# Kernel tuning notes

Measured on AMD Instinct MI355X. Metric: run time of the kernel, lower is better.

The kernel has to match this reference:

```python
import math
import jax, jax.numpy as jnp
import numpy as np

HEADS = 8
D_MODEL = 256


def positional_encoding_2d(c, h, w):
    # faithful port of wzlxjtu/PositionalEncoding2D
    d = c // 2
    div_term = jnp.exp(jnp.arange(0.0, d, 2, dtype=jnp.float32) * (-(math.log(10000.0) / d)))  # [d//2? no: d/2 entries -> d//2]
    pos_w = jnp.arange(0.0, w, dtype=jnp.float32)[:, None] * div_term  # [w, d//2]
    pos_h = jnp.arange(0.0, h, dtype=jnp.float32)[:, None] * div_term  # [h, d//2]
    pe = jnp.zeros((c, h, w), dtype=jnp.float32)
    sw = jnp.broadcast_to(jnp.sin(pos_w).T[:, None, :], (div_term.shape[0], h, w))
    cw = jnp.broadcast_to(jnp.cos(pos_w).T[:, None, :], (div_term.shape[0], h, w))
    sh = jnp.broadcast_to(jnp.sin(pos_h).T[:, :, None], (div_term.shape[0], h, w))
    ch = jnp.broadcast_to(jnp.cos(pos_h).T[:, :, None], (div_term.shape[0], h, w))
    pe = pe.at[0:d:2].set(sw)
    pe = pe.at[1:d:2].set(cw)
    pe = pe.at[d::2].set(sh)
    pe = pe.at[d + 1::2].set(ch)
    return pe


def setup_inputs() -> dict:
    key = jax.random.key(0)
    ks = jax.random.split(key, 9)
    b, c, h, w = 2, D_MODEL, 64, 64
    x = jax.random.normal(ks[0], (b, c, h, w), dtype=jnp.float32)
    s = 0.02
    Wq = jax.random.normal(ks[1], (c, c), dtype=jnp.float32) * s
    Wk = jax.random.normal(ks[2], (c, c), dtype=jnp.float32) * s
    Wv = jax.random.normal(ks[3], (c, c), dtype=jnp.float32) * s
    Wo = jax.random.normal(ks[4], (c, c), dtype=jnp.float32) * s
    bq = jax.random.normal(ks[5], (c,), dtype=jnp.float32) * s
    bk = jax.random.normal(ks[6], (c,), dtype=jnp.float32) * s
    bv = jax.random.normal(ks[7], (c,), dtype=jnp.float32) * s
    bo = jax.random.normal(ks[8], (c,), dtype=jnp.float32) * s
    return {"x": x, "Wq": Wq, "bq": bq, "Wk": Wk, "bk": bk,
            "Wv": Wv, "bv": bv, "Wo": Wo, "bo": bo}


def reference(x, Wq, bq, Wk, bk, Wv, bv, Wo, bo):
    b, c, h, w = x.shape
    dk = c // HEADS
    pe = positional_encoding_2d(c, h, w)
    x2 = x + pe[None]                                   # [b,c,h,w]
    tok = x2.reshape(b, c, h * w).transpose(0, 2, 1)    # [b,N,c]
    q = (tok @ Wq.T + bq).reshape(b, -1, HEADS, dk).transpose(0, 2, 1, 3)  # [b,H,N,dk]
    k = (tok @ Wk.T + bk).reshape(b, -1, HEADS, dk).transpose(0, 2, 1, 3)
    v = (tok @ Wv.T + bv).reshape(b, -1, HEADS, dk).transpose(0, 2, 1, 3)
    scores = jnp.einsum('bhnd,bhmd->bhnm', q, k) / math.sqrt(dk)  # [b,H,N,N]
    attn = jax.nn.softmax(scores, axis=-1)
    out = jnp.einsum('bhnm,bhmd->bhnd', attn, v)        # [b,H,N,dk]
    concat = out.transpose(0, 2, 1, 3).reshape(b, -1, c)  # [b,N,c]
    proj = concat @ Wo.T + bo                           # [b,N,c]
    return proj.transpose(0, 2, 1).reshape(b, c, h, w)
```

## Files before the change

### kernel.cpp

```cpp
#include <hip/hip_runtime.h>
#include <hip/hip_bf16.h>
#include <cstdint>

typedef float f32x4 __attribute__((ext_vector_type(4)));
typedef __bf16 bf16x8 __attribute__((ext_vector_type(8)));
typedef uint32_t uint2v __attribute__((ext_vector_type(2)));

#define MFMA_K32(A, B, C) __builtin_amdgcn_mfma_f32_16x16x32_bf16((A), (B), (C), 0, 0, 0)

#if __has_builtin(__builtin_amdgcn_exp2f)
#define EXP2(x) __builtin_amdgcn_exp2f(x)
#else
#define EXP2(x) exp2f(x)
#endif

static __device__ __forceinline__ uint16_t f2b(float f) {
    uint32_t u = __float_as_uint(f);
    uint32_t r = (u + 0x7fffu + ((u >> 16) & 1u)) >> 16;
    return (uint16_t)r;
}

static __device__ __forceinline__ uint32_t packbf(float a, float b) {
    uint32_t r;
    asm("v_cvt_pk_bf16_f32 %0, %1, %2" : "=v"(r) : "v"(a), "v"(b));
    return r;
}

__global__ __launch_bounds__(512) void prep(const float* __restrict__ x,
                                            const float* __restrict__ wq,
                                            const float* __restrict__ wk,
                                            const float* __restrict__ wv,
                                            const float* __restrict__ wo,
                                            uint16_t* __restrict__ dst,
                                            uint16_t* __restrict__ tok) {
    __shared__ uint16_t T[64][65];
    int tid = threadIdx.x, bid = blockIdx.x;
    if (bid < 512) {
        int nt = bid & 63, ct = (bid >> 6) & 3, bb = bid >> 8;
        int n0 = nt << 6, c0 = ct << 6;
        int nl = tid & 63, cq = tid >> 6;
        int n = n0 + nl;
        float pf = (float)((c0 & 128) ? nt : nl);
        int cbase = c0 + cq * 8;
        int ibase = (cbase & 127) >> 1;
        float dt = __expf((float)(2 * ibase) * -0.07195578415606394f);
#pragma unroll
        for (int j = 0; j < 4; ++j) {
            float sv, cv;
            __sincosf(pf * dt, &sv, &cv);
            int cl = cq * 8 + 2 * j;
            int cc = cbase + 2 * j;
            T[cl][nl]     = f2b(x[((size_t)(bb * 256 + cc) << 12) + n] + sv);
            T[cl + 1][nl] = f2b(x[((size_t)(bb * 256 + cc + 1) << 12) + n] + cv);
            dt *= 0.8659643233600653f;
        }
        __syncthreads();
#pragma unroll
        for (int p = 0; p < 8; ++p) {
            int tl = cq * 8 + p;
            tok[(((size_t)(bb << 12) | (n0 + tl)) << 8) + c0 + nl] = T[nl][tl];
        }
    } else {
        int idx = (bid - 512) * 512 + tid;
        int which = idx >> 16, off = idx & 65535;
        const float* s = (which == 0) ? wq : (which == 1) ? wk : (which == 2) ? wv : wo;
        dst[idx] = f2b(s[off]);
    }
}

__global__ __launch_bounds__(256) void qkv_gemm(const uint16_t* __restrict__ tok,
                                                const uint16_t* __restrict__ Wall,
                                                const float* __restrict__ bq,
                                                const float* __restrict__ bk,
                                                const float* __restrict__ bv,
                                                uint16_t* __restrict__ qo,
                                                uint16_t* __restrict__ ko,
                                                uint16_t* __restrict__ vo) {
    __shared__ __align__(16) uint16_t WS[64][264];
    int tid = threadIdx.x, wv = tid >> 6, lane = tid & 63;
    int c16 = lane & 15, quad = lane >> 4;
    int M0 = blockIdx.x * 64 + wv * 16;
    int O0 = blockIdx.y * 64;
    const uint16_t* arow = tok + (size_t)(M0 + c16) * 256;
    bf16x8 af[8];
#pragma unroll
    for (int kk = 0; kk < 8; ++kk) af[kk] = *(const bf16x8*)(arow + kk * 32 + quad * 8);
    f32x4 zero = {0.f, 0.f, 0.f, 0.f};
    int bb = M0 >> 12, n = (M0 + c16) & 4095;
    int srow = tid >> 5, sch = (tid & 31) << 3;
    for (int mat = 0; mat < 3; ++mat) {
        const uint16_t* Wg = Wall + (size_t)mat * 65536 + (size_t)O0 * 256;
        __syncthreads();
#pragma unroll
        for (int p = 0; p < 8; ++p)
            *(bf16x8*)(&WS[p * 8 + srow][sch]) = *(const bf16x8*)(Wg + (p * 8 + srow) * 256 + sch);
        __syncthreads();
        f32x4 acc[4] = {zero, zero, zero, zero};
#pragma unroll
        for (int kk = 0; kk < 8; ++kk) {
            int k0 = kk * 32 + quad * 8;
#pragma unroll
            for (int nb = 0; nb < 4; ++nb)
                acc[nb] = MFMA_K32(*(const bf16x8*)(&WS[nb * 16 + c16][k0]),
                                   af[kk], acc[nb]);
        }
        const float* bias = (mat == 0) ? bq : (mat == 1) ? bk : bv;
        if (mat < 2) {
            float scale = (mat == 0) ? 0.25505654134660127f : 1.0f;
            uint16_t* dst = (mat == 0) ? qo : ko;
#pragma unroll
            for (int nb = 0; nb < 4; ++nb) {
                int o = O0 + nb * 16 + quad * 4;
                f32x4 bi = *(const f32x4*)(bias + o);
                int h = o >> 5, dd = o & 31;
                uint2v pk;
                pk[0] = packbf((acc[nb][0] + bi[0]) * scale, (acc[nb][1] + bi[1]) * scale);
                pk[1] = packbf((acc[nb][2] + bi[2]) * scale, (acc[nb][3] + bi[3]) * scale);
                *(uint2v*)(dst + ((size_t)(bb * 8 + h) * 4096 + n) * 32 + dd) = pk;
            }
        } else {
#pragma unroll
            for (int nb = 0; nb < 4; ++nb)
#pragma unroll
                for (int r = 0; r < 4; ++r) {
                    int o = O0 + nb * 16 + quad * 4 + r;
                    vo[((size_t)(bb * 8 + (o >> 5)) * 32 + (o & 31)) * 4096 + n] =
                        f2b(acc[nb][r] + bias[o]);
                }
        }
    }
}

__global__ __launch_bounds__(512, 2) void flash(const uint16_t* __restrict__ qb,
                                                const uint16_t* __restrict__ kb,
                                                const uint16_t* __restrict__ vtb,
                                                uint16_t* __restrict__ concat) {
    __shared__ __align__(16) char smem[38912];
    int tid = threadIdx.x, wv = tid >> 6, lane = tid & 63;
    int c16 = lane & 15, quad = lane >> 4;
    int half = tid >> 8, t2 = tid & 255;
    int bh = blockIdx.y;
    int q0 = (blockIdx.x << 8) + (wv & 3) * 64;
    size_t base = (size_t)bh << 12;

    uint16_t* KT = (uint16_t*)(smem + half * 19456);
    uint16_t* VT = (uint16_t*)(smem + half * 19456 + 10240);

    const uint16_t* kgp = kb + (base + (size_t)half * 2048 + (t2 >> 2)) * 32 + (t2 & 3) * 8;
    const uint16_t* vgp = vtb + ((size_t)bh * 32 + (t2 >> 3)) * 4096 + half * 2048 + (t2 & 7) * 8;
    uint16_t* kls = KT + (t2 >> 2) * 40 + (t2 & 3) * 8;
    uint16_t* vls = VT + (t2 >> 3) * 72 + (t2 & 7) * 8;

    bf16x8 qf[4];
#pragma unroll
    for (int qbk = 0; qbk < 4; ++qbk)
        qf[qbk] = *(const bf16x8*)(qb + (base + q0 + qbk * 16 + c16) * 32 + quad * 8);

    int rbase = ((c16 >> 2) << 3) + (c16 & 3);

    union { uint32_t u[4]; bf16x8 v; } onesu;
    onesu.u[0] = 0x3F803F80u; onesu.u[1] = 0x3F803F80u;
    onesu.u[2] = 0x3F803F80u; onesu.u[3] = 0x3F803F80u;
    bf16x8 ones = onesu.v;

    f32x4 zero = {0.f, 0.f, 0.f, 0.f};
    f32x4 oA[4], oB[4], oS[4];
#pragma unroll
    for (int qbk = 0; qbk < 4; ++qbk) { oA[qbk] = zero; oB[qbk] = zero; oS[qbk] = zero; }

    {
        bf16x8 kr = *(const bf16x8*)kgp;
        bf16x8 vr = *(const bf16x8*)vgp;
        *(bf16x8*)kls = kr;
        *(bf16x8*)vls = vr;
    }
    __syncthreads();

    for (int kt = 0; kt < 32; ++kt) {
        int cur = kt & 1;
        int kn = (kt + 1) & 31;
        bf16x8 kr = *(const bf16x8*)(kgp + (size_t)kn * 2048);
        bf16x8 vr = *(const bf16x8*)(vgp + kn * 64);
        const uint16_t* kfp = KT + cur * 2560 + rbase * 40 + quad * 8;
        const uint16_t* vfp = VT + cur * 2304 + c16 * 72 + quad * 8;
        bf16x8 kf[4], vA[2], vB[2];
        kf[0] = *(const bf16x8*)(kfp);
        kf[1] = *(const bf16x8*)(kfp + 160);
        kf[2] = *(const bf16x8*)(kfp + 1280);
        kf[3] = *(const bf16x8*)(kfp + 1440);
        vA[0] = *(const bf16x8*)(vfp);
        vA[1] = *(const bf16x8*)(vfp + 32);
        vB[0] = *(const bf16x8*)(vfp + 1152);
        vB[1] = *(const bf16x8*)(vfp + 1152 + 32);

#pragma unroll
        for (int qbk = 0; qbk < 4; ++qbk) {
            f32x4 s[4];
#pragma unroll
            for (int c = 0; c < 4; ++c) s[c] = MFMA_K32(kf[c], qf[qbk], zero);
#pragma unroll
            for (int p = 0; p < 2; ++p) {
#pragma unroll
                for (int r = 0; r < 4; ++r) {
                    s[2 * p][r] = EXP2(s[2 * p][r]);
                    s[2 * p + 1][r] = EXP2(s[2 * p + 1][r]);
                }
                union { bf16x8 v; uint32_t u[4]; } pa;
                pa.u[0] = packbf(s[2 * p][0], s[2 * p][1]);
                pa.u[1] = packbf(s[2 * p][2], s[2 * p][3]);
                pa.u[2] = packbf(s[2 * p + 1][0], s[2 * p + 1][1]);
                pa.u[3] = packbf(s[2 * p + 1][2], s[2 * p + 1][3]);
                oA[qbk] = MFMA_K32(pa.v, vA[p], oA[qbk]);
                oB[qbk] = MFMA_K32(pa.v, vB[p], oB[qbk]);
                oS[qbk] = MFMA_K32(pa.v, ones, oS[qbk]);
            }
        }

        *(bf16x8*)(kls + (cur ^ 1) * 2560) = kr;
        *(bf16x8*)(vls + (cur ^ 1) * 2304) = vr;
        __syncthreads();
    }

    float* ov = (float*)smem;
    if (wv >= 4) {
        float* d = ov + ((wv - 4) * 64 + lane) * 33;
#pragma unroll
        for (int qbk = 0; qbk < 4; ++qbk)
#pragma unroll
            for (int r = 0; r < 4; ++r) {
                d[qbk * 8 + r] = oA[qbk][r];
                d[qbk * 8 + 4 + r] = oB[qbk][r];
            }
    }
    __syncthreads();
    if (wv < 4) {
        const float* s = ov + (wv * 64 + lane) * 33;
#pragma unroll
        for (int qbk = 0; qbk < 4; ++qbk)
#pragma unroll
            for (int r = 0; r < 4; ++r) {
                oA[qbk][r] += s[qbk * 8 + r];
                oB[qbk][r] += s[qbk * 8 + 4 + r];
            }
    }
    __syncthreads();
    if (wv >= 4) {
        float* d = ov + ((wv - 4) * 64 + lane) * 17;
#pragma unroll
        for (int qbk = 0; qbk < 4; ++qbk)
#pragma unroll
            for (int r = 0; r < 4; ++r) d[qbk * 4 + r] = oS[qbk][r];
    }
    __syncthreads();
    if (wv < 4) {
        const float* s = ov + (wv * 64 + lane) * 17;
        int h = bh & 7, bb = bh >> 3;
#pragma unroll
        for (int qbk = 0; qbk < 4; ++qbk)
#pragma unroll
            for (int r = 0; r < 4; ++r) {
                float l = oS[qbk][r] + s[qbk * 4 + r];
                float inv = 1.f / l;
                int n = q0 + qbk * 16 + quad * 4 + r;
                size_t row = ((size_t)bb * 4096 + n) * 256 + h * 32;
                concat[row + c16]      = f2b(oA[qbk][r] * inv);
                concat[row + 16 + c16] = f2b(oB[qbk][r] * inv);
            }
    }
}

__global__ __launch_bounds__(256) void proj_gemm(const uint16_t* __restrict__ concat,
                                                 const uint16_t* __restrict__ Wo,
                                                 const float* __restrict__ bo,
                                                 float* __restrict__ out) {
    __shared__ __align__(16) uint16_t WS[64][264];
    int tid = threadIdx.x, wv = tid >> 6, lane = tid & 63;
    int c16 = lane & 15, quad = lane >> 4;
    int M0 = blockIdx.x * 64 + wv * 16;
    int O0 = blockIdx.y * 64;
    int srow = tid >> 5, sch = (tid & 31) << 3;
    const uint16_t* Wg = Wo + (size_t)O0 * 256;
#pragma unroll
    for (int p = 0; p < 8; ++p)
        *(bf16x8*)(&WS[p * 8 + srow][sch]) = *(const bf16x8*)(Wg + (p * 8 + srow) * 256 + sch);
    const uint16_t* crow = concat + (size_t)(M0 + c16) * 256;
    bf16x8 af[8];
#pragma unroll
    for (int kk = 0; kk < 8; ++kk) af[kk] = *(const bf16x8*)(crow + kk * 32 + quad * 8);
    __syncthreads();
    f32x4 zero = {0.f, 0.f, 0.f, 0.f};
    f32x4 acc[4] = {zero, zero, zero, zero};
#pragma unroll
    for (int kk = 0; kk < 8; ++kk) {
        int k0 = kk * 32 + quad * 8;
#pragma unroll
        for (int nb = 0; nb < 4; ++nb)
            acc[nb] = MFMA_K32(*(const bf16x8*)(&WS[nb * 16 + c16][k0]),
                               af[kk], acc[nb]);
    }
    int bb = M0 >> 12, n = (M0 + c16) & 4095;
#pragma unroll
    for (int nb = 0; nb < 4; ++nb)
#pragma unroll
        for (int r = 0; r < 4; ++r) {
            int o = O0 + nb * 16 + quad * 4 + r;
            out[((size_t)(bb * 256 + o) << 12) + n] = acc[nb][r] + bo[o];
        }
}

extern "C" void kernel_launch(void* const* d_in, const int* in_sizes, int n_in,
                              void* d_out, int out_size, void* d_ws, size_t ws_size,
                              hipStream_t stream) {
    const float* x  = (const float*)d_in[0];
    const float* Wq = (const float*)d_in[1];
    const float* bq = (const float*)d_in[2];
    const float* Wk = (const float*)d_in[3];
    const float* bk = (const float*)d_in[4];
    const float* Wv = (const float*)d_in[5];
    const float* bv = (const float*)d_in[6];
    const float* Wo = (const float*)d_in[7];
    const float* bo = (const float*)d_in[8];
    float* out = (float*)d_out;

    uint16_t* ws   = (uint16_t*)d_ws;
    uint16_t* Wb   = ws;
    uint16_t* tok  = Wb + 4 * 65536;
    uint16_t* q    = tok + 2097152;
    uint16_t* k    = q + 2097152;
    uint16_t* vt   = k + 2097152;
    uint16_t* cc   = vt + 2097152;

    prep<<<1024, 512, 0, stream>>>(x, Wq, Wk, Wv, Wo, Wb, tok);
    qkv_gemm<<<dim3(128, 4), 256, 0, stream>>>(tok, Wb, bq, bk, bv, q, k, vt);
    flash<<<dim3(16, 16), 512, 0, stream>>>(q, k, vt, cc);
    proj_gemm<<<dim3(128, 4), 256, 0, stream>>>(cc, Wb + 3 * 65536, bo, out);
}
```

Measured before the change: 144.5 us.

## Split flash attention KV loop four ways and halve queries per block

```diff
diff --git a/kernel.cpp b/kernel.cpp
--- a/kernel.cpp
+++ b/kernel.cpp
@@ -131,25 +131,28 @@
     }
 }
 
-__global__ __launch_bounds__(512, 2) void flash(const uint16_t* __restrict__ qb,
+__global__ __launch_bounds__(512, 4) void flash(const uint16_t* __restrict__ qb,
                                                 const uint16_t* __restrict__ kb,
                                                 const uint16_t* __restrict__ vtb,
                                                 uint16_t* __restrict__ concat) {
-    __shared__ __align__(16) char smem[38912];
+    __shared__ __align__(16) char smem[77824];
     int tid = threadIdx.x, wv = tid >> 6, lane = tid & 63;
     int c16 = lane & 15, quad = lane >> 4;
-    int half = tid >> 8, t2 = tid & 255;
+    int kq = tid >> 7, t2 = tid & 127;
     int bh = blockIdx.y;
-    int q0 = (blockIdx.x << 8) + (wv & 3) * 64;
+    int qg = wv & 1;
+    int q0 = (blockIdx.x << 7) + qg * 64;
     size_t base = (size_t)bh << 12;
 
-    uint16_t* KT = (uint16_t*)(smem + half * 19456);
-    uint16_t* VT = (uint16_t*)(smem + half * 19456 + 10240);
-
-    const uint16_t* kgp = kb + (base + (size_t)half * 2048 + (t2 >> 2)) * 32 + (t2 & 3) * 8;
-    const uint16_t* vgp = vtb + ((size_t)bh * 32 + (t2 >> 3)) * 4096 + half * 2048 + (t2 & 7) * 8;
-    uint16_t* kls = KT + (t2 >> 2) * 40 + (t2 & 3) * 8;
-    uint16_t* vls = VT + (t2 >> 3) * 72 + (t2 & 7) * 8;
+    uint16_t* KTg = (uint16_t*)(smem + kq * 19456);
+    uint16_t* VTg = KTg + 5120;
+    const uint16_t* kgp = kb + (base + (size_t)kq * 1024 + (t2 >> 2)) * 32 + (t2 & 3) * 8;
+    const uint16_t* vgp = vtb + ((size_t)bh * 32 + (t2 >> 3)) * 4096 + kq * 1024 + (t2 & 7) * 8;
+    uint16_t* kls = KTg + (t2 >> 2) * 40 + (t2 & 3) * 8;
+    uint16_t* vls = VTg + (t2 >> 3) * 72 + (t2 & 7) * 8;
+
+    uint16_t* KTw = (uint16_t*)(smem + (wv >> 1) * 19456);
+    uint16_t* VTw = KTw + 5120;
 
     bf16x8 qf[4];
 #pragma unroll
@@ -169,20 +172,26 @@
     for (int qbk = 0; qbk < 4; ++qbk) { oA[qbk] = zero; oB[qbk] = zero; oS[qbk] = zero; }
 
     {
-        bf16x8 kr = *(const bf16x8*)kgp;
-        bf16x8 vr = *(const bf16x8*)vgp;
-        *(bf16x8*)kls = kr;
-        *(bf16x8*)vls = vr;
+        bf16x8 k0 = *(const bf16x8*)kgp;
+        bf16x8 k1 = *(const bf16x8*)(kgp + 1024);
+        bf16x8 v0 = *(const bf16x8*)vgp;
+        bf16x8 v1 = *(const bf16x8*)(vgp + (size_t)16 * 4096);
+        *(bf16x8*)kls = k0;
+        *(bf16x8*)(kls + 1280) = k1;
+        *(bf16x8*)vls = v0;
+        *(bf16x8*)(vls + 1152) = v1;
     }
     __syncthreads();
 
-    for (int kt = 0; kt < 32; ++kt) {
+    for (int kt = 0; kt < 16; ++kt) {
         int cur = kt & 1;
-        int kn = (kt + 1) & 31;
-        bf16x8 kr = *(const bf16x8*)(kgp + (size_t)kn * 2048);
-        bf16x8 vr = *(const bf16x8*)(vgp + kn * 64);
-        const uint16_t* kfp = KT + cur * 2560 + rbase * 40 + quad * 8;
-        const uint16_t* vfp = VT + cur * 2304 + c16 * 72 + quad * 8;
+        int kn = (kt + 1) & 15;
+        bf16x8 k0 = *(const bf16x8*)(kgp + (size_t)kn * 2048);
+        bf16x8 k1 = *(const bf16x8*)(kgp + (size_t)kn * 2048 + 1024);
+        bf16x8 v0 = *(const bf16x8*)(vgp + kn * 64);
+        bf16x8 v1 = *(const bf16x8*)(vgp + (size_t)16 * 4096 + kn * 64);
+        const uint16_t* kfp = KTw + cur * 2560 + rbase * 40 + quad * 8;
+        const uint16_t* vfp = VTw + cur * 2304 + c16 * 72 + quad * 8;
         bf16x8 kf[4], vA[2], vB[2];
         kf[0] = *(const bf16x8*)(kfp);
         kf[1] = *(const bf16x8*)(kfp + 160);
@@ -216,51 +225,45 @@
             }
         }
 
-        *(bf16x8*)(kls + (cur ^ 1) * 2560) = kr;
-        *(bf16x8*)(vls + (cur ^ 1) * 2304) = vr;
+        *(bf16x8*)(kls + (cur ^ 1) * 2560) = k0;
+        *(bf16x8*)(kls + (cur ^ 1) * 2560 + 1280) = k1;
+        *(bf16x8*)(vls + (cur ^ 1) * 2304) = v0;
+        *(bf16x8*)(vls + (cur ^ 1) * 2304 + 1152) = v1;
         __syncthreads();
     }
 
     float* ov = (float*)smem;
-    if (wv >= 4) {
-        float* d = ov + ((wv - 4) * 64 + lane) * 33;
+    if (wv >= 2) {
+        float* d = ov + ((wv - 2) * 64 + lane) * 49;
 #pragma unroll
         for (int qbk = 0; qbk < 4; ++qbk)
 #pragma unroll
             for (int r = 0; r < 4; ++r) {
-                d[qbk * 8 + r] = oA[qbk][r];
-                d[qbk * 8 + 4 + r] = oB[qbk][r];
+                d[qbk * 12 + r]     = oA[qbk][r];
+                d[qbk * 12 + 4 + r] = oB[qbk][r];
+                d[qbk * 12 + 8 + r] = oS[qbk][r];
             }
     }
     __syncthreads();
-    if (wv < 4) {
-        const float* s = ov + (wv * 64 + lane) * 33;
+    if (wv < 2) {
+#pragma unroll
+        for (int j = 0; j < 3; ++j) {
+            const float* s = ov + ((wv + 2 * j) * 64 + lane) * 49;
+#pragma unroll
+            for (int qbk = 0; qbk < 4; ++qbk)
+#pragma unroll
+                for (int r = 0; r < 4; ++r) {
+                    oA[qbk][r] += s[qbk * 12 + r];
+                    oB[qbk][r] += s[qbk * 12 + 4 + r];
+                    oS[qbk][r] += s[qbk * 12 + 8 + r];
+                }
+        }
+        int h = bh & 7, bb = bh >> 3;
 #pragma unroll
         for (int qbk = 0; qbk < 4; ++qbk)
 #pragma unroll
             for (int r = 0; r < 4; ++r) {
-                oA[qbk][r] += s[qbk * 8 + r];
-                oB[qbk][r] += s[qbk * 8 + 4 + r];
-            }
-    }
-    __syncthreads();
-    if (wv >= 4) {
-        float* d = ov + ((wv - 4) * 64 + lane) * 17;
-#pragma unroll
-        for (int qbk = 0; qbk < 4; ++qbk)
-#pragma unroll
-            for (int r = 0; r < 4; ++r) d[qbk * 4 + r] = oS[qbk][r];
-    }
-    __syncthreads();
-    if (wv < 4) {
-        const float* s = ov + (wv * 64 + lane) * 17;
-        int h = bh & 7, bb = bh >> 3;
-#pragma unroll
-        for (int qbk = 0; qbk < 4; ++qbk)
-#pragma unroll
-            for (int r = 0; r < 4; ++r) {
-                float l = oS[qbk][r] + s[qbk * 4 + r];
-                float inv = 1.f / l;
+                float inv = 1.f / oS[qbk][r];
                 int n = q0 + qbk * 16 + quad * 4 + r;
                 size_t row = ((size_t)bb * 4096 + n) * 256 + h * 32;
                 concat[row + c16]      = f2b(oA[qbk][r] * inv);
@@ -332,6 +335,6 @@
 
     prep<<<1024, 512, 0, stream>>>(x, Wq, Wk, Wv, Wo, Wb, tok);
     qkv_gemm<<<dim3(128, 4), 256, 0, stream>>>(tok, Wb, bq, bk, bv, q, k, vt);
-    flash<<<dim3(16, 16), 512, 0, stream>>>(q, k, vt, cc);
+    flash<<<dim3(32, 16), 512, 0, stream>>>(q, k, vt, cc);
     proj_gemm<<<dim3(128, 4), 256, 0, stream>>>(cc, Wb + 3 * 65536, bo, out);
 }
```

Measured after the change: 132.5 us, median of 2. -8.3%, faster.
